# Optimization experiments

Measured on AMD Instinct MI355X. Metric: run time of the kernel, lower is better.

The kernel has to match this reference:

```python
import jax, jax.numpy as jnp
import numpy as np

IN_CHANNELS = 128
KERNEL = 3

def setup_inputs() -> dict:
    key = jax.random.key(0)
    k1, k2, k3 = jax.random.split(key, 3)
    B, C, L = 32, IN_CHANNELS, 8192
    inputs = jax.random.normal(k1, (B, C, L), dtype=jnp.float32)
    # per-channel Conv1d(1,1,k=3) weights/biases; PyTorch init U(-1/sqrt(3), 1/sqrt(3))
    bound = 1.0 / np.sqrt(KERNEL)
    weight = jax.random.uniform(k2, (C, KERNEL), dtype=jnp.float32, minval=-bound, maxval=bound)
    bias = jax.random.uniform(k3, (C,), dtype=jnp.float32, minval=-bound, maxval=bound)
    return {"inputs": inputs, "weight": weight, "bias": bias}

def reference(inputs, weight, bias):
    # Depthwise conv1d, kernel=3, stride=1, padding=1 (cross-correlation like torch Conv1d).
    B, C, L = inputs.shape
    xp = jnp.pad(inputs, ((0, 0), (0, 0), (1, 1)))  # [B, C, L+2]
    # out[b,c,l] = sum_k weight[c,k] * xp[b,c,l+k] + bias[c]
    out = (weight[None, :, 0:1] * xp[:, :, 0:L]
           + weight[None, :, 1:2] * xp[:, :, 1:L + 1]
           + weight[None, :, 2:3] * xp[:, :, 2:L + 2]
           + bias[None, :, None])
    return out
```

## Files before the change

kernel.cpp:

```cpp
#include <hip/hip_runtime.h>


constexpr int C  = 128;
constexpr int L  = 8192;
constexpr int L4 = L / 4;
constexpr int B  = 32;
constexpr int TOTAL4 = B * C * L4;

constexpr int BLOCK  = 256;
constexpr int GRID   = 2048;
constexpr int STRIDE = BLOCK * GRID;
constexpr int ITER   = TOTAL4 / STRIDE;
constexpr int BATCH  = 4;

static_assert(TOTAL4 % STRIDE == 0, "exact tiling");
static_assert((STRIDE / L4) % C == 0, "channel invariant across iterations");

typedef float floatx4 __attribute__((ext_vector_type(4)));

__global__ __launch_bounds__(BLOCK) void dwconv1d_kernel(
    const float4* __restrict__ x4,
    const float* __restrict__ x,
    const float* __restrict__ w,
    const float* __restrict__ bias,
    float4* __restrict__ out4)
{
    const int idx0 = blockIdx.x * BLOCK + threadIdx.x;
    const int lane = threadIdx.x & 63;
    const int i4   = idx0 & (L4 - 1);

    const int c = __builtin_amdgcn_readfirstlane((idx0 >> 11) & (C - 1));
    const float w0 = w[c * 3 + 0];
    const float w1 = w[c * 3 + 1];
    const float w2 = w[c * 3 + 2];
    const float bc = bias[c];

    const bool lane0    = (lane == 0);
    const bool lane63   = (lane == 63);
    const bool rowstart = (i4 == 0);
    const bool rowend   = (i4 == L4 - 1);

    #pragma unroll
    for (int jo = 0; jo < ITER / BATCH; ++jo) {
        int    idx[BATCH];
        float4 v[BATCH];

        #pragma unroll
        for (int ji = 0; ji < BATCH; ++ji) {
            idx[ji] = idx0 + (jo * BATCH + ji) * STRIDE;
            v[ji]   = x4[idx[ji]];
        }

        #pragma unroll
        for (int ji = 0; ji < BATCH; ++ji) {
            const float4 vv = v[ji];

            float left  = __shfl_up(vv.w, 1);
            float right = __shfl_down(vv.x, 1);

            const long base = (long)idx[ji] * 4;
            if (lane0)  left  = rowstart ? 0.0f : x[base - 1];
            if (lane63) right = rowend   ? 0.0f : x[base + 4];

            floatx4 o;
            o.x = fmaf(w0, left,  fmaf(w1, vv.x, fmaf(w2, vv.y, bc)));
            o.y = fmaf(w0, vv.x,  fmaf(w1, vv.y, fmaf(w2, vv.z, bc)));
            o.z = fmaf(w0, vv.y,  fmaf(w1, vv.z, fmaf(w2, vv.w, bc)));
            o.w = fmaf(w0, vv.z,  fmaf(w1, vv.w, fmaf(w2, right, bc)));

            __builtin_nontemporal_store(o, (floatx4*)&out4[idx[ji]]);
        }
    }
}

extern "C" void kernel_launch(void* const* d_in, const int* in_sizes, int n_in,
                              void* d_out, int out_size, void* d_ws, size_t ws_size,
                              hipStream_t stream)
{
    const float* x    = (const float*)d_in[0];
    const float* w    = (const float*)d_in[1];
    const float* bias = (const float*)d_in[2];
    float* out        = (float*)d_out;

    dwconv1d_kernel<<<GRID, BLOCK, 0, stream>>>(
        (const float4*)x, x, w, bias, (float4*)out);
}
```

Baseline: 237.1 us.

## Replace grid-stride loop with one-shot blocks and use regular stores

The persistent grid-stride kernel (2048 blocks, 32 items per thread) becomes a one-shot launch where each block handles a contiguous chunk of 1024 float4s, with 4 loads per thread issued up front. The output store also changes from a nontemporal store to a plain store. The aim is to cut loop overhead and let the hardware scheduler spread many small blocks across CUs. In exchange there is one wave of launch and scheduling work per block, and plain stores may pollute the cache.

```diff
diff --git a/kernel.cpp b/kernel.cpp
--- a/kernel.cpp
+++ b/kernel.cpp
@@ -7,16 +7,13 @@
 constexpr int B  = 32;
 constexpr int TOTAL4 = B * C * L4;
 
-constexpr int BLOCK  = 256;
-constexpr int GRID   = 2048;
-constexpr int STRIDE = BLOCK * GRID;
-constexpr int ITER   = TOTAL4 / STRIDE;
-constexpr int BATCH  = 4;
+constexpr int BLOCK = 256;
+constexpr int BATCH = 4;
+constexpr int ITEMS_PER_BLOCK = BLOCK * BATCH;
+constexpr int GRID  = TOTAL4 / ITEMS_PER_BLOCK;
 
-static_assert(TOTAL4 % STRIDE == 0, "exact tiling");
-static_assert((STRIDE / L4) % C == 0, "channel invariant across iterations");
-
-typedef float floatx4 __attribute__((ext_vector_type(4)));
+static_assert(TOTAL4 % ITEMS_PER_BLOCK == 0, "exact tiling");
+static_assert(L4 % ITEMS_PER_BLOCK == 0, "block never spans a row boundary");
 
 __global__ __launch_bounds__(BLOCK) void dwconv1d_kernel(
     const float4* __restrict__ x4,
@@ -25,9 +22,9 @@
     const float* __restrict__ bias,
     float4* __restrict__ out4)
 {
-    const int idx0 = blockIdx.x * BLOCK + threadIdx.x;
-    const int lane = threadIdx.x & 63;
-    const int i4   = idx0 & (L4 - 1);
+    const int tid  = threadIdx.x;
+    const int lane = tid & 63;
+    const int idx0 = blockIdx.x * ITEMS_PER_BLOCK + tid;
 
     const int c = __builtin_amdgcn_readfirstlane((idx0 >> 11) & (C - 1));
     const float w0 = w[c * 3 + 0];
@@ -35,41 +32,34 @@
     const float w2 = w[c * 3 + 2];
     const float bc = bias[c];
 
-    const bool lane0    = (lane == 0);
-    const bool lane63   = (lane == 63);
-    const bool rowstart = (i4 == 0);
-    const bool rowend   = (i4 == L4 - 1);
+    const bool lane0  = (lane == 0);
+    const bool lane63 = (lane == 63);
+
+    float4 v[BATCH];
+    #pragma unroll
+    for (int ji = 0; ji < BATCH; ++ji)
+        v[ji] = x4[idx0 + ji * BLOCK];
 
     #pragma unroll
-    for (int jo = 0; jo < ITER / BATCH; ++jo) {
-        int    idx[BATCH];
-        float4 v[BATCH];
+    for (int ji = 0; ji < BATCH; ++ji) {
+        const int idx = idx0 + ji * BLOCK;
+        const int i4  = idx & (L4 - 1);
+        const float4 vv = v[ji];
 
-        #pragma unroll
-        for (int ji = 0; ji < BATCH; ++ji) {
-            idx[ji] = idx0 + (jo * BATCH + ji) * STRIDE;
-            v[ji]   = x4[idx[ji]];
-        }
+        float left  = __shfl_up(vv.w, 1);
+        float right = __shfl_down(vv.x, 1);
 
-        #pragma unroll
-        for (int ji = 0; ji < BATCH; ++ji) {
-            const float4 vv = v[ji];
+        const long base = (long)idx * 4;
+        if (lane0)  left  = (i4 == 0)      ? 0.0f : x[base - 1];
+        if (lane63) right = (i4 == L4 - 1) ? 0.0f : x[base + 4];
 
-            float left  = __shfl_up(vv.w, 1);
-            float right = __shfl_down(vv.x, 1);
+        float4 o;
+        o.x = fmaf(w0, left,  fmaf(w1, vv.x, fmaf(w2, vv.y, bc)));
+        o.y = fmaf(w0, vv.x,  fmaf(w1, vv.y, fmaf(w2, vv.z, bc)));
+        o.z = fmaf(w0, vv.y,  fmaf(w1, vv.z, fmaf(w2, vv.w, bc)));
+        o.w = fmaf(w0, vv.z,  fmaf(w1, vv.w, fmaf(w2, right, bc)));
 
-            const long base = (long)idx[ji] * 4;
-            if (lane0)  left  = rowstart ? 0.0f : x[base - 1];
-            if (lane63) right = rowend   ? 0.0f : x[base + 4];
-
-            floatx4 o;
-            o.x = fmaf(w0, left,  fmaf(w1, vv.x, fmaf(w2, vv.y, bc)));
-            o.y = fmaf(w0, vv.x,  fmaf(w1, vv.y, fmaf(w2, vv.z, bc)));
-            o.z = fmaf(w0, vv.y,  fmaf(w1, vv.z, fmaf(w2, vv.w, bc)));
-            o.w = fmaf(w0, vv.z,  fmaf(w1, vv.w, fmaf(w2, right, bc)));
-
-            __builtin_nontemporal_store(o, (floatx4*)&out4[idx[ji]]);
-        }
+        out4[idx] = o;
     }
 }
 
```

Result: no change. 233.1 us (-1.7%).
